# Kernel optimization log

Measured on AMD Instinct MI355X. Metric: run time of the kernel, lower is better.

The kernel has to match this reference:

```python
import jax, jax.numpy as jnp
import numpy as np

T, B, IN, H, OUT = 2048, 64, 32, 512, 32


def setup_inputs() -> dict:
    key = jax.random.key(0)
    ks = jax.random.split(key, 7)
    s = 1.0 / np.sqrt(H)
    return {
        "inputs": jax.random.normal(ks[0], (T, B, IN), dtype=jnp.float32),
        "h0": jnp.zeros((B, H), dtype=jnp.float32),
        "c0": jnp.zeros((B, H), dtype=jnp.float32),
        "W_ih": jax.random.uniform(ks[1], (4 * H, IN), minval=-s, maxval=s, dtype=jnp.float32),
        "W_hh": jax.random.uniform(ks[2], (4 * H, H), minval=-s, maxval=s, dtype=jnp.float32),
        "b_ih": jax.random.uniform(ks[3], (4 * H,), minval=-s, maxval=s, dtype=jnp.float32),
        "b_hh": jax.random.uniform(ks[4], (4 * H,), minval=-s, maxval=s, dtype=jnp.float32),
        "W_out": jax.random.uniform(ks[5], (OUT, H), minval=-s, maxval=s, dtype=jnp.float32),
        "b_out": jax.random.uniform(ks[6], (OUT,), minval=-s, maxval=s, dtype=jnp.float32),
    }


def reference(inputs, h0, c0, W_ih, W_hh, b_ih, b_hh, W_out, b_out):
    Hh = h0.shape[-1]
    # Precompute input projections for all timesteps: [T, B, 4H]
    x_proj = jnp.einsum('tbi,gi->tbg', inputs, W_ih) + b_ih + b_hh

    def step(carry, xp):
        h, c = carry
        gates = xp + h @ W_hh.T  # [B, 4H]
        i, f, g, o = jnp.split(gates, 4, axis=-1)  # torch LSTMCell gate order
        i = jax.nn.sigmoid(i)
        f = jax.nn.sigmoid(f)
        g = jnp.tanh(g)
        o = jax.nn.sigmoid(o)
        c_new = f * c + i * g
        h_new = o * jnp.tanh(c_new)
        return (h_new, c_new), h_new

    (h_T, c_T), h_all = jax.lax.scan(step, (h0, c0), x_proj)
    outputs = jnp.einsum('tbh,oh->tbo', h_all, W_out) + b_out  # [T, B, OUT]
    return outputs, (h_T, c_T)
```

## Files before the change

### kernel.cpp

```cpp
#include <hip/hip_runtime.h>

#define TT 2048
#define BB 64
#define INF 32
#define HH 512
#define OO 32

typedef __attribute__((ext_vector_type(8))) short bf16x8;
typedef __attribute__((ext_vector_type(4))) float f32x4;

__device__ __forceinline__ float sigm(float x) {
  return 1.f / (1.f + __expf(-x));
}
__device__ __forceinline__ float tanh_(float x) {
  float e = __expf(2.f * x);
  return 1.f - 2.f / (1.f + e);
}
__device__ __forceinline__ unsigned short f2bf(float f) {
  unsigned u = __float_as_uint(f);
  u = (u + 0x7FFFu + ((u >> 16) & 1u)) >> 16;
  return (unsigned short)u;
}
__device__ __forceinline__ float bf2f(unsigned short s) {
  return __uint_as_float(((unsigned)s) << 16);
}

#define COH_LOAD4(dst, ptr)                                                  \
  asm volatile("global_load_dwordx4 %0, %1, off sc0 sc1"                     \
               : "=v"(dst) : "v"(ptr))

#define SPIN_LIMIT 20000

#define HSTR 528

__global__ __launch_bounds__(512, 2)
void lstm_fused(const float* __restrict__ X,
                const float* __restrict__ h0,
                const float* __restrict__ c0,
                const float* __restrict__ Wih,
                const float* __restrict__ Whh,
                const float* __restrict__ bih,
                const float* __restrict__ bhh,
                const float* __restrict__ Wout,
                const float* __restrict__ bout,
                float* __restrict__ outp,
                float* __restrict__ hT,
                float* __restrict__ cT,
                unsigned short* __restrict__ hring,
                int* __restrict__ flags)
{
  const int tid    = threadIdx.x;
  const int rg     = tid >> 6;
  const int lane   = tid & 63;
  const int bg     = blockIdx.x & 7;
  const int sl     = blockIdx.x >> 3;
  const int bglob0 = bg << 3;

  __shared__ float gsh[512];
  __shared__ __align__(16) unsigned short hlds[8 * HSTR];

  const bool mwave = (rg < 4);

  bf16x8 aW[16], aX;
  float biasf[4];
  if (mwave) {
    const int arow = (rg << 9) + (sl << 4) + (lane & 15);
    const float* wb = Whh + (size_t)arow * HH + ((lane >> 4) << 3);
#pragma unroll
    for (int kt = 0; kt < 16; ++kt) {
      float4 a = ((const float4*)(wb + kt * 32))[0];
      float4 b = ((const float4*)(wb + kt * 32))[1];
      bf16x8 f;
      f[0] = (short)f2bf(a.x); f[1] = (short)f2bf(a.y);
      f[2] = (short)f2bf(a.z); f[3] = (short)f2bf(a.w);
      f[4] = (short)f2bf(b.x); f[5] = (short)f2bf(b.y);
      f[6] = (short)f2bf(b.z); f[7] = (short)f2bf(b.w);
      aW[kt] = f;
    }
    const float* wi = Wih + (size_t)arow * INF + ((lane >> 4) << 3);
    float4 a = ((const float4*)wi)[0];
    float4 b = ((const float4*)wi)[1];
    aX[0] = (short)f2bf(a.x); aX[1] = (short)f2bf(a.y);
    aX[2] = (short)f2bf(a.z); aX[3] = (short)f2bf(a.w);
    aX[4] = (short)f2bf(b.x); aX[5] = (short)f2bf(b.y);
    aX[6] = (short)f2bf(b.z); aX[7] = (short)f2bf(b.w);
#pragma unroll
    for (int r = 0; r < 4; ++r) {
      int rrow = (rg << 9) + (sl << 4) + ((lane >> 4) << 2) + r;
      biasf[r] = bih[rrow] + bhh[rrow];
    }
  }
  float wout[8];
  {
    const float4* wp = (const float4*)(Wout + sl * HH + (lane << 3));
    float4 a = wp[0], b4 = wp[1];
    wout[0] = a.x;  wout[1] = a.y;  wout[2] = a.z;  wout[3] = a.w;
    wout[4] = b4.x; wout[5] = b4.y; wout[6] = b4.z; wout[7] = b4.w;
  }
  const float bo = bout[sl];

  const int ojj = tid >> 3, ob = tid & 7;
  const int hoff_owner = (bglob0 + ob) * HH + (sl << 4) + ojj;
  float cst = (tid < 128) ? c0[hoff_owner] : 0.f;

  const int lb = tid >> 6, lg = tid & 63;
  int* myflags = flags + (bg << 5);

  for (int t = 0; t < TT; ++t) {
    float4 xva, xvb;
    if (mwave) {
      const float* xr = X + (size_t)t * BB * INF + (bglob0 + (lane & 7)) * INF
                        + ((lane >> 4) << 3);
      xva = ((const float4*)xr)[0];
      xvb = ((const float4*)xr)[1];
    }

    if (t > 0 && rg == 0) {
      int f = __hip_atomic_load(&myflags[lane & 31], __ATOMIC_RELAXED,
                                __HIP_MEMORY_SCOPE_AGENT);
      int guard = 0;
      while (__any(f < t)) {
        if (++guard > SPIN_LIMIT) break;
        __builtin_amdgcn_s_sleep(1);
        f = __hip_atomic_load(&myflags[lane & 31], __ATOMIC_RELAXED,
                              __HIP_MEMORY_SCOPE_AGENT);
      }
    }
    __syncthreads();

    if (t == 0) {
      const float* hp = h0 + (size_t)(bglob0 + lb) * HH + (lg << 3);
      float4 a = ((const float4*)hp)[0];
      float4 b = ((const float4*)hp)[1];
      unsigned d0 = (unsigned)f2bf(a.x) | ((unsigned)f2bf(a.y) << 16);
      unsigned d1 = (unsigned)f2bf(a.z) | ((unsigned)f2bf(a.w) << 16);
      unsigned d2 = (unsigned)f2bf(b.x) | ((unsigned)f2bf(b.y) << 16);
      unsigned d3 = (unsigned)f2bf(b.z) | ((unsigned)f2bf(b.w) << 16);
      *(int4*)(hlds + lb * HSTR + (lg << 3)) = make_int4(d0, d1, d2, d3);
    } else {
      const unsigned short* hsrc = hring + (size_t)((t - 1) & 1) * BB * HH
                                   + (size_t)(bglob0 + lb) * HH + (lg << 3);
      int4 hv;
      COH_LOAD4(hv, hsrc);
      asm volatile("s_waitcnt vmcnt(0)" ::: "memory");
      __builtin_amdgcn_sched_barrier(0);
      *(int4*)(hlds + lb * HSTR + (lg << 3)) = hv;
    }
    __syncthreads();

    if (mwave) {
      f32x4 acc = {0.f, 0.f, 0.f, 0.f};
      bf16x8 bx;
      bx[0] = (short)f2bf(xva.x); bx[1] = (short)f2bf(xva.y);
      bx[2] = (short)f2bf(xva.z); bx[3] = (short)f2bf(xva.w);
      bx[4] = (short)f2bf(xvb.x); bx[5] = (short)f2bf(xvb.y);
      bx[6] = (short)f2bf(xvb.z); bx[7] = (short)f2bf(xvb.w);
      acc = __builtin_amdgcn_mfma_f32_16x16x32_bf16(aX, bx, acc, 0, 0, 0);
      const unsigned short* hb = hlds + (lane & 7) * HSTR + ((lane >> 4) << 3);
#pragma unroll
      for (int kt = 0; kt < 16; ++kt) {
        bf16x8 bf = *(const bf16x8*)(hb + kt * 32);
        acc = __builtin_amdgcn_mfma_f32_16x16x32_bf16(aW[kt], bf, acc, 0, 0, 0);
      }
      if ((lane & 15) < 8) {
        const int gb = (rg << 7) + ((lane >> 4) << 5) + (lane & 15);
#pragma unroll
        for (int r = 0; r < 4; ++r)
          gsh[gb + (r << 3)] = acc[r] + biasf[r];
      }
    } else {
      const int wb2 = (rg - 4) << 1;
      const bf16x8 ha = *(const bf16x8*)(hlds + wb2 * HSTR + (lane << 3));
      const bf16x8 hc = *(const bf16x8*)(hlds + (wb2 + 1) * HSTR + (lane << 3));
      float o0 = 0.f, o1 = 0.f;
#pragma unroll
      for (int j = 0; j < 8; ++j) {
        o0 = __fmaf_rn(bf2f((unsigned short)ha[j]), wout[j], o0);
        o1 = __fmaf_rn(bf2f((unsigned short)hc[j]), wout[j], o1);
      }
#pragma unroll
      for (int s = 32; s >= 1; s >>= 1) {
        o0 += __shfl_xor(o0, s, 64);
        o1 += __shfl_xor(o1, s, 64);
      }
      if (t > 0 && lane == 0) {
        outp[(size_t)(t - 1) * BB * OO + (bglob0 + wb2) * OO + sl] = o0 + bo;
        outp[(size_t)(t - 1) * BB * OO + (bglob0 + wb2 + 1) * OO + sl] = o1 + bo;
      }
    }
    __syncthreads();

    if (tid < 128) {
      float gi = gsh[(ojj << 3) + ob];
      float gf = gsh[128 + (ojj << 3) + ob];
      float gg = gsh[256 + (ojj << 3) + ob];
      float go = gsh[384 + (ojj << 3) + ob];
      float i_ = sigm(gi), f_ = sigm(gf), g_ = tanh_(gg), o_ = sigm(go);
      cst = __fmaf_rn(f_, cst, i_ * g_);
      float hv = o_ * tanh_(cst);
      float hv2 = __shfl(hv, (lane + 8) & 63, 64);
      if ((lane & 8) == 0) {
        unsigned pk = (unsigned)f2bf(hv) | ((unsigned)f2bf(hv2) << 16);
        unsigned* slot32 = (unsigned*)(hring + (size_t)(t & 1) * BB * HH);
        __hip_atomic_store(&slot32[((bglob0 + ob) << 8) + (sl << 3) + (ojj >> 1)],
                           pk, __ATOMIC_RELAXED, __HIP_MEMORY_SCOPE_AGENT);
      }
      if (t == TT - 1) { hT[hoff_owner] = hv; cT[hoff_owner] = cst; }
    }
    __syncthreads();
    if (tid == 0)
      __hip_atomic_store(&myflags[sl], t + 1, __ATOMIC_RELAXED,
                         __HIP_MEMORY_SCOPE_AGENT);
  }

  if (rg == 0) {
    int f = __hip_atomic_load(&myflags[lane & 31], __ATOMIC_RELAXED,
                              __HIP_MEMORY_SCOPE_AGENT);
    int guard = 0;
    while (__any(f < TT)) {
      if (++guard > SPIN_LIMIT) break;
      __builtin_amdgcn_s_sleep(1);
      f = __hip_atomic_load(&myflags[lane & 31], __ATOMIC_RELAXED,
                            __HIP_MEMORY_SCOPE_AGENT);
    }
  }
  __syncthreads();
  {
    const unsigned short* hb = hring + (size_t)((TT - 1) & 1) * BB * HH
                               + (size_t)(bglob0 + rg) * HH + (lane << 3);
    int4 p;
    COH_LOAD4(p, hb);
    asm volatile("s_waitcnt vmcnt(0)" ::: "memory");
    __builtin_amdgcn_sched_barrier(0);
    float oacc =
        __uint_as_float(((unsigned)p.x) << 16)        * wout[0] +
        __uint_as_float(((unsigned)p.x) & 0xFFFF0000u) * wout[1] +
        __uint_as_float(((unsigned)p.y) << 16)        * wout[2] +
        __uint_as_float(((unsigned)p.y) & 0xFFFF0000u) * wout[3] +
        __uint_as_float(((unsigned)p.z) << 16)        * wout[4] +
        __uint_as_float(((unsigned)p.z) & 0xFFFF0000u) * wout[5] +
        __uint_as_float(((unsigned)p.w) << 16)        * wout[6] +
        __uint_as_float(((unsigned)p.w) & 0xFFFF0000u) * wout[7];
#pragma unroll
    for (int s = 32; s >= 1; s >>= 1) oacc += __shfl_xor(oacc, s, 64);
    if (lane == 0)
      outp[(size_t)(TT - 1) * BB * OO + (bglob0 + rg) * OO + sl] = oacc + bo;
  }
}

extern "C" void kernel_launch(void* const* d_in, const int* in_sizes, int n_in,
                              void* d_out, int out_size, void* d_ws, size_t ws_size,
                              hipStream_t stream) {
  const float* X    = (const float*)d_in[0];
  const float* h0   = (const float*)d_in[1];
  const float* c0   = (const float*)d_in[2];
  const float* Wih  = (const float*)d_in[3];
  const float* Whh  = (const float*)d_in[4];
  const float* bih  = (const float*)d_in[5];
  const float* bhh  = (const float*)d_in[6];
  const float* Wout = (const float*)d_in[7];
  const float* bout = (const float*)d_in[8];

  float* outp = (float*)d_out;
  float* hT   = outp + (size_t)TT * BB * OO;
  float* cT   = hT + (size_t)BB * HH;

  unsigned short* hring = (unsigned short*)d_ws;
  int* flags = (int*)((char*)d_ws + (size_t)2 * BB * HH * sizeof(unsigned short));

  hipMemsetAsync(flags, 0, 8 * 32 * sizeof(int), stream);

  lstm_fused<<<dim3(256), dim3(512), 0, stream>>>(
      X, h0, c0, Wih, Whh, bih, bhh, Wout, bout, outp, hT, cT, hring, flags);
}
```

Before: 4.396 ms.

## Permute W_hh rows so each MFMA lane holds all four gates, fusing cell update

The rows of W_hh loaded into each MFMA wave are remapped so that the four accumulator registers of a lane hold the i, f, g, o gates for the same hidden unit. The LSTM cell update then runs directly in registers, which removes the shared-memory gate buffer and one block-wide barrier per timestep on the serial recurrence path. The output-projection stores are also moved to after the flag publish so they sit off the critical path. In exchange, activation math is done redundantly by lanes that are not owners, and the index mapping becomes more intricate.

```diff
diff --git a/kernel.cpp b/kernel.cpp
--- a/kernel.cpp
+++ b/kernel.cpp
@@ -56,7 +56,6 @@
   const int sl     = blockIdx.x >> 3;
   const int bglob0 = bg << 3;
 
-  __shared__ float gsh[512];
   __shared__ __align__(16) unsigned short hlds[8 * HSTR];
 
   const bool mwave = (rg < 4);
@@ -64,7 +63,8 @@
   bf16x8 aW[16], aX;
   float biasf[4];
   if (mwave) {
-    const int arow = (rg << 9) + (sl << 4) + (lane & 15);
+    const int ri = lane & 15;
+    const int arow = ((ri & 3) << 9) + (sl << 4) + (rg << 2) + (ri >> 2);
     const float* wb = Whh + (size_t)arow * HH + ((lane >> 4) << 3);
 #pragma unroll
     for (int kt = 0; kt < 16; ++kt) {
@@ -86,8 +86,8 @@
     aX[6] = (short)f2bf(b.z); aX[7] = (short)f2bf(b.w);
 #pragma unroll
     for (int r = 0; r < 4; ++r) {
-      int rrow = (rg << 9) + (sl << 4) + ((lane >> 4) << 2) + r;
-      biasf[r] = bih[rrow] + bhh[rrow];
+      int grow = (r << 9) + (sl << 4) + (rg << 2) + (lane >> 4);
+      biasf[r] = bih[grow] + bhh[grow];
     }
   }
   float wout[8];
@@ -99,9 +99,11 @@
   }
   const float bo = bout[sl];
 
-  const int ojj = tid >> 3, ob = tid & 7;
+  const bool owner = mwave && ((lane & 15) < 8);
+  const int ob = lane & 7;
+  const int ojj = (rg << 2) + (lane >> 4);
   const int hoff_owner = (bglob0 + ob) * HH + (sl << 4) + ojj;
-  float cst = (tid < 128) ? c0[hoff_owner] : 0.f;
+  float cst = owner ? c0[hoff_owner] : 0.f;
 
   const int lb = tid >> 6, lg = tid & 63;
   int* myflags = flags + (bg << 5);
@@ -148,6 +150,7 @@
     }
     __syncthreads();
 
+    float o0 = 0.f, o1 = 0.f;
     if (mwave) {
       f32x4 acc = {0.f, 0.f, 0.f, 0.f};
       bf16x8 bx;
@@ -162,17 +165,26 @@
         bf16x8 bf = *(const bf16x8*)(hb + kt * 32);
         acc = __builtin_amdgcn_mfma_f32_16x16x32_bf16(aW[kt], bf, acc, 0, 0, 0);
       }
-      if ((lane & 15) < 8) {
-        const int gb = (rg << 7) + ((lane >> 4) << 5) + (lane & 15);
-#pragma unroll
-        for (int r = 0; r < 4; ++r)
-          gsh[gb + (r << 3)] = acc[r] + biasf[r];
-      }
+      float i_ = sigm(acc[0] + biasf[0]);
+      float f_ = sigm(acc[1] + biasf[1]);
+      float g_ = tanh_(acc[2] + biasf[2]);
+      float o_ = sigm(acc[3] + biasf[3]);
+      float cnew = __fmaf_rn(f_, cst, i_ * g_);
+      float hv = o_ * tanh_(cnew);
+      if (owner) cst = cnew;
+      float hv2 = __shfl(hv, (lane + 16) & 63, 64);
+      if (owner && ((lane >> 4) & 1) == 0) {
+        unsigned pk = (unsigned)f2bf(hv) | ((unsigned)f2bf(hv2) << 16);
+        unsigned* slot32 = (unsigned*)(hring + (size_t)(t & 1) * BB * HH);
+        __hip_atomic_store(
+            &slot32[((bglob0 + ob) << 8) + (sl << 3) + (rg << 1) + (lane >> 5)],
+            pk, __ATOMIC_RELAXED, __HIP_MEMORY_SCOPE_AGENT);
+      }
+      if (owner && t == TT - 1) { hT[hoff_owner] = hv; cT[hoff_owner] = cst; }
     } else {
       const int wb2 = (rg - 4) << 1;
       const bf16x8 ha = *(const bf16x8*)(hlds + wb2 * HSTR + (lane << 3));
       const bf16x8 hc = *(const bf16x8*)(hlds + (wb2 + 1) * HSTR + (lane << 3));
-      float o0 = 0.f, o1 = 0.f;
 #pragma unroll
       for (int j = 0; j < 8; ++j) {
         o0 = __fmaf_rn(bf2f((unsigned short)ha[j]), wout[j], o0);
@@ -183,34 +195,16 @@
         o0 += __shfl_xor(o0, s, 64);
         o1 += __shfl_xor(o1, s, 64);
       }
-      if (t > 0 && lane == 0) {
-        outp[(size_t)(t - 1) * BB * OO + (bglob0 + wb2) * OO + sl] = o0 + bo;
-        outp[(size_t)(t - 1) * BB * OO + (bglob0 + wb2 + 1) * OO + sl] = o1 + bo;
-      }
-    }
-    __syncthreads();
-
-    if (tid < 128) {
-      float gi = gsh[(ojj << 3) + ob];
-      float gf = gsh[128 + (ojj << 3) + ob];
-      float gg = gsh[256 + (ojj << 3) + ob];
-      float go = gsh[384 + (ojj << 3) + ob];
-      float i_ = sigm(gi), f_ = sigm(gf), g_ = tanh_(gg), o_ = sigm(go);
-      cst = __fmaf_rn(f_, cst, i_ * g_);
-      float hv = o_ * tanh_(cst);
-      float hv2 = __shfl(hv, (lane + 8) & 63, 64);
-      if ((lane & 8) == 0) {
-        unsigned pk = (unsigned)f2bf(hv) | ((unsigned)f2bf(hv2) << 16);
-        unsigned* slot32 = (unsigned*)(hring + (size_t)(t & 1) * BB * HH);
-        __hip_atomic_store(&slot32[((bglob0 + ob) << 8) + (sl << 3) + (ojj >> 1)],
-                           pk, __ATOMIC_RELAXED, __HIP_MEMORY_SCOPE_AGENT);
-      }
-      if (t == TT - 1) { hT[hoff_owner] = hv; cT[hoff_owner] = cst; }
     }
     __syncthreads();
     if (tid == 0)
       __hip_atomic_store(&myflags[sl], t + 1, __ATOMIC_RELAXED,
                          __HIP_MEMORY_SCOPE_AGENT);
+    if (!mwave && t > 0 && lane == 0) {
+      const int wb2 = (rg - 4) << 1;
+      outp[(size_t)(t - 1) * BB * OO + (bglob0 + wb2) * OO + sl] = o0 + bo;
+      outp[(size_t)(t - 1) * BB * OO + (bglob0 + wb2 + 1) * OO + sl] = o1 + bo;
+    }
   }
 
   if (rg == 0) {
```

New measurement: 4.122 ms. 1.07x faster.
